# Kernel tuning notes

Measured on AMD Instinct MI355X. Metric: run time of the kernel, lower is better.

Reference implementation:

```python
import jax, jax.numpy as jnp
import numpy as np

IN_SIZE = 1024
OUT_SIZE = 4096
LOGN = 12          # ceil(log2(max(in,out)))
N = 1 << LOGN      # 4096
BATCH = 8192


def setup_inputs() -> dict:
    key = jax.random.key(0)
    k1, k2, k3 = jax.random.split(key, 3)
    # kaiming_uniform on [2*logN, N]: fan_in = N, bound = sqrt(6/fan_in)
    bound = float(np.sqrt(6.0 / N))
    learned_params = jax.random.uniform(k1, (2 * LOGN, N), minval=-bound, maxval=bound, dtype=jnp.float32)
    inp = jax.random.normal(k2, (BATCH, IN_SIZE), dtype=jnp.float32)
    # np.random.permutation(N)[:out_size]
    out_row_indices = jax.random.permutation(k3, N)[:OUT_SIZE].astype(jnp.int32)
    return {"input": inp, "learned_params": learned_params, "out_row_indices": out_row_indices}


def reference(input, learned_params, out_row_indices):
    # Build B = prod_i (diag(p[2i]) + P_i @ diag(p[2i+1])), P_i[j, j^2^i] = 1.
    # (P_i @ diag(d) @ B)[j, :] = d[j^2^i] * B[j^2^i, :], so each layer is a
    # row-scale + xor-permuted row-scale of B (same math as the dense matmul chain).
    B = jnp.eye(N, dtype=input.dtype)
    for i in range(LOGN):
        perm = jnp.arange(N) ^ (1 << i)  # static per layer
        B = learned_params[2 * i][:, None] * B + learned_params[2 * i + 1][perm][:, None] * B[perm]
    layer_matrix = B[out_row_indices, :IN_SIZE]   # [out_size, in_size]
    return input @ layer_matrix.T                  # [batch, out_size]
```

## Files before the change

### kernel.cpp

```cpp
#include <hip/hip_runtime.h>


typedef float f4 __attribute__((ext_vector_type(4)));
typedef float f2 __attribute__((ext_vector_type(2)));
typedef int   i4 __attribute__((ext_vector_type(4)));

__device__ __forceinline__ int swz(int e) {
    return e ^ (((e >> 5) & 3) << 2);
}

template<int CTRL>
__device__ __forceinline__ float dppx(float x) {
    int xi = __builtin_bit_cast(int, x);
    int r  = __builtin_amdgcn_update_dpp(xi, xi, CTRL, 0xF, 0xF, true);
    return __builtin_bit_cast(float, r);
}

#if __has_builtin(__builtin_amdgcn_permlane16_swap) && __has_builtin(__builtin_amdgcn_permlane32_swap)
#define HAVE_PERMLANE_SWAP 1
__device__ __forceinline__ float xswap16(float x) {
    unsigned xi = __builtin_bit_cast(unsigned, x);
    auto r = __builtin_amdgcn_permlane16_swap(xi, xi, false, false);
    return __builtin_bit_cast(float, r[0] ^ r[1] ^ xi);
}
__device__ __forceinline__ float xswap32(float x) {
    unsigned xi = __builtin_bit_cast(unsigned, x);
    auto r = __builtin_amdgcn_permlane32_swap(xi, xi, false, false);
    return __builtin_bit_cast(float, r[0] ^ r[1] ^ xi);
}
#else
#define HAVE_PERMLANE_SWAP 0
__device__ __forceinline__ float xswap16(float x) { return __shfl_xor(x, 16, 64); }
__device__ __forceinline__ float xswap32(float x) { return __shfl_xor(x, 32, 64); }
#endif

__global__ void __launch_bounds__(256) bfly_prep(
    const float* __restrict__ lp, const int* __restrict__ orow,
    float* __restrict__ scale, int* __restrict__ src2)
{
    int j = blockIdx.x * 256 + threadIdx.x;
    if (j >= 4096) return;
    int r = orow[j];
    int c = r & 1023;
    int u = r & 2047;
    const float* A10 = lp + 20 * 4096;
    const float* B10 = lp + 21 * 4096;
    const float* A11 = lp + 22 * 4096;
    const float* B11 = lp + 23 * 4096;
    float f11 = (r & 2048) ? B11[u] : A11[u];
    float f10 = (r & 1024) ? B10[c] : A10[c];
    scale[j] = f11 * f10;
    src2[j] = c ^ (((c >> 4) & 7) << 1);
}

__global__ void __launch_bounds__(512, 2) bfly_main(
    const float* __restrict__ inp, const float* __restrict__ lp,
    const float* __restrict__ scale, const int* __restrict__ src2,
    float* __restrict__ out)
{
    __shared__ __align__(16) float cf[20 * 1024 + 8 * 2048];
    const int t = threadIdx.x;
    const int wave = t >> 6, lane = t & 63;

    #pragma unroll
    for (int step = 0; step < 10; ++step) {
        const int q = 2 * step + (t >> 8);
        const int e = (t & 255) * 4;
        const f4 v = *reinterpret_cast<const f4*>(lp + (size_t)q * 4096 + e);
        *reinterpret_cast<f4*>(&cf[q * 1024 + swz(e)]) = v;
    }

    const int sBase = blockIdx.x * 16 + wave * 2;
    float x[2][16];
    #pragma unroll
    for (int m = 0; m < 2; ++m) {
        const f4* p = reinterpret_cast<const f4*>(inp + (size_t)(sBase + m) * 1024 + lane * 16);
        #pragma unroll
        for (int c = 0; c < 4; ++c) {
            f4 v = p[c];
            x[m][4*c+0] = v.x; x[m][4*c+1] = v.y; x[m][4*c+2] = v.z; x[m][4*c+3] = v.w;
        }
    }

    __syncthreads();

    #pragma unroll
    for (int i = 0; i < 2; ++i) {
        const float* arow = &cf[(size_t)(2*i)     * 1024];
        const float* brow = &cf[(size_t)(2*i + 1) * 1024];
        #pragma unroll
        for (int c = 0; c < 4; ++c) {
            f4 va = *reinterpret_cast<const f4*>(&arow[swz(lane * 16 + 4 * c)]);
            f4 vb = *reinterpret_cast<const f4*>(&brow[swz(lane * 16 + 4 * c)]);
            #pragma unroll
            for (int m = 0; m < 2; ++m) {
                float* xm = x[m];
                if (i == 0) {
                    float lo0 = xm[4*c+0], hi0 = xm[4*c+1];
                    xm[4*c+0] = va[0] * lo0 + vb[1] * hi0;
                    xm[4*c+1] = va[1] * hi0 + vb[0] * lo0;
                    float lo1 = xm[4*c+2], hi1 = xm[4*c+3];
                    xm[4*c+2] = va[2] * lo1 + vb[3] * hi1;
                    xm[4*c+3] = va[3] * hi1 + vb[2] * lo1;
                } else {
                    float lo0 = xm[4*c+0], hi0 = xm[4*c+2];
                    xm[4*c+0] = va[0] * lo0 + vb[2] * hi0;
                    xm[4*c+2] = va[2] * hi0 + vb[0] * lo0;
                    float lo1 = xm[4*c+1], hi1 = xm[4*c+3];
                    xm[4*c+1] = va[1] * lo1 + vb[3] * hi1;
                    xm[4*c+3] = va[3] * hi1 + vb[1] * lo1;
                }
            }
        }
    }

    #pragma unroll
    for (int i = 2; i < 4; ++i) {
        const float* arow = &cf[(size_t)(2*i)     * 1024];
        const float* brow = &cf[(size_t)(2*i + 1) * 1024];
        #pragma unroll
        for (int g = 0; g < 2; ++g) {
            const int q0 = (i == 2) ? 2 * g : g;
            const int q1 = (i == 2) ? q0 + 1 : q0 + 2;
            f4 va0 = *reinterpret_cast<const f4*>(&arow[swz(lane * 16 + 4 * q0)]);
            f4 va1 = *reinterpret_cast<const f4*>(&arow[swz(lane * 16 + 4 * q1)]);
            f4 vb0 = *reinterpret_cast<const f4*>(&brow[swz(lane * 16 + 4 * q0)]);
            f4 vb1 = *reinterpret_cast<const f4*>(&brow[swz(lane * 16 + 4 * q1)]);
            #pragma unroll
            for (int m = 0; m < 2; ++m) {
                float* xm = x[m];
                #pragma unroll
                for (int e = 0; e < 4; ++e) {
                    float lo = xm[4*q0+e], hi = xm[4*q1+e];
                    xm[4*q0+e] = va0[e] * lo + vb1[e] * hi;
                    xm[4*q1+e] = va1[e] * hi + vb0[e] * lo;
                }
            }
        }
    }

    {
        const float* arow = &cf[(size_t)8 * 1024];
        const float* brow = &cf[(size_t)9 * 1024];
        #pragma unroll
        for (int c = 0; c < 4; ++c) {
            f4 va = *reinterpret_cast<const f4*>(&arow[swz(lane * 16 + 4 * c)]);
            f4 vb = *reinterpret_cast<const f4*>(&brow[swz((lane ^ 1) * 16 + 4 * c)]);
            #pragma unroll
            for (int m = 0; m < 2; ++m) {
                #pragma unroll
                for (int e = 0; e < 4; ++e) {
                    float v = x[m][4*c+e];
                    x[m][4*c+e] = va[e] * v + vb[e] * dppx<0xB1>(v);
                }
            }
        }
    }

    #pragma unroll
    for (int i = 5; i < 10; ++i) {
        const int d = 1 << (i - 4);
        const float* arow = &cf[(size_t)(2*i)     * 1024];
        const float* brow = &cf[(size_t)(2*i + 1) * 1024];
        #pragma unroll
        for (int c = 0; c < 4; ++c) {
            f4 va = *reinterpret_cast<const f4*>(&arow[swz(lane * 16 + 4 * c)]);
            f4 vb = *reinterpret_cast<const f4*>(&brow[swz((lane ^ d) * 16 + 4 * c)]);
            #pragma unroll
            for (int m = 0; m < 2; ++m) {
                #pragma unroll
                for (int e = 0; e < 4; ++e) {
                    float v = x[m][4*c+e];
                    float xp = (d == 2)  ? dppx<0x4E>(v)
                             : (d == 8)  ? dppx<0x128>(v)
                             : (d == 16) ? xswap16(v)
                             : (d == 32) ? xswap32(v)
                             :             __shfl_xor(v, d, 64);
                    x[m][4*c+e] = va[e] * v + vb[e] * xp;
                }
            }
        }
    }

    float* zz = &cf[20 * 1024 + (size_t)wave * 2048];
    const int km0 = (lane & 7) << 1;
    #pragma unroll
    for (int k = 0; k < 16; k += 2) {
        int pi = lane * 16 + (k ^ km0);
        f4 v = { x[0][k], x[1][k], x[0][k+1], x[1][k+1] };
        *reinterpret_cast<f4*>(&zz[2 * pi]) = v;
    }

    const i4* srv = reinterpret_cast<const i4*>(src2);
    const f4* scv = reinterpret_cast<const f4*>(scale);
    f4* o0 = reinterpret_cast<f4*>(out + (size_t)sBase * 4096);
    f4* o1 = reinterpret_cast<f4*>(out + (size_t)(sBase + 1) * 4096);

    i4 si = srv[lane];
    f4 sc = scv[lane];
    #pragma unroll
    for (int it = 0; it < 16; ++it) {
        i4 si_c = si;
        f4 sc_c = sc;
        if (it + 1 < 16) {
            si = srv[(it + 1) * 64 + lane];
            sc = scv[(it + 1) * 64 + lane];
        }
        int j4 = it * 64 + lane;
        f2 vx = *reinterpret_cast<const f2*>(&zz[2 * si_c.x]);
        f2 vy = *reinterpret_cast<const f2*>(&zz[2 * si_c.y]);
        f2 vz = *reinterpret_cast<const f2*>(&zz[2 * si_c.z]);
        f2 vw = *reinterpret_cast<const f2*>(&zz[2 * si_c.w]);
        f4 r0 = { sc_c.x * vx.x, sc_c.y * vy.x, sc_c.z * vz.x, sc_c.w * vw.x };
        f4 r1 = { sc_c.x * vx.y, sc_c.y * vy.y, sc_c.z * vz.y, sc_c.w * vw.y };
        o0[j4] = r0;
        o1[j4] = r1;
    }
}

extern "C" void kernel_launch(void* const* d_in, const int* in_sizes, int n_in,
                              void* d_out, int out_size, void* d_ws, size_t ws_size,
                              hipStream_t stream) {
    const float* inp  = (const float*)d_in[0];
    const float* lp   = (const float*)d_in[1];
    const int*   orow = (const int*)d_in[2];
    float* out = (float*)d_out;

    float* scale = (float*)d_ws;
    int*   src2  = (int*)((char*)d_ws + 4096 * 4);

    bfly_prep<<<16, 256, 0, stream>>>(lp, orow, scale, src2);
    bfly_main<<<512, 512, 0, stream>>>(inp, lp, scale, src2, out);
}
```

Baseline: 41.76 us.

## Process four rows per wave with 256-thread blocks and f4 gather staging

After: 46.16 us. 1.11x slower.

```diff
diff --git a/kernel.cpp b/kernel.cpp
--- a/kernel.cpp
+++ b/kernel.cpp
@@ -2,7 +2,6 @@
 
 
 typedef float f4 __attribute__((ext_vector_type(4)));
-typedef float f2 __attribute__((ext_vector_type(2)));
 typedef int   i4 __attribute__((ext_vector_type(4)));
 
 __device__ __forceinline__ int swz(int e) {
@@ -17,7 +16,6 @@
 }
 
 #if __has_builtin(__builtin_amdgcn_permlane16_swap) && __has_builtin(__builtin_amdgcn_permlane32_swap)
-#define HAVE_PERMLANE_SWAP 1
 __device__ __forceinline__ float xswap16(float x) {
     unsigned xi = __builtin_bit_cast(unsigned, x);
     auto r = __builtin_amdgcn_permlane16_swap(xi, xi, false, false);
@@ -29,14 +27,13 @@
     return __builtin_bit_cast(float, r[0] ^ r[1] ^ xi);
 }
 #else
-#define HAVE_PERMLANE_SWAP 0
 __device__ __forceinline__ float xswap16(float x) { return __shfl_xor(x, 16, 64); }
 __device__ __forceinline__ float xswap32(float x) { return __shfl_xor(x, 32, 64); }
 #endif
 
 __global__ void __launch_bounds__(256) bfly_prep(
     const float* __restrict__ lp, const int* __restrict__ orow,
-    float* __restrict__ scale, int* __restrict__ src2)
+    float* __restrict__ scale, int* __restrict__ src4)
 {
     int j = blockIdx.x * 256 + threadIdx.x;
     if (j >= 4096) return;
@@ -50,30 +47,29 @@
     float f11 = (r & 2048) ? B11[u] : A11[u];
     float f10 = (r & 1024) ? B10[c] : A10[c];
     scale[j] = f11 * f10;
-    src2[j] = c ^ (((c >> 4) & 7) << 1);
-}
-
-__global__ void __launch_bounds__(512, 2) bfly_main(
+    src4[j] = c ^ ((c >> 4) & 7);
+}
+
+__global__ void __launch_bounds__(256, 1) bfly_main(
     const float* __restrict__ inp, const float* __restrict__ lp,
-    const float* __restrict__ scale, const int* __restrict__ src2,
+    const float* __restrict__ scale, const int* __restrict__ src4,
     float* __restrict__ out)
 {
-    __shared__ __align__(16) float cf[20 * 1024 + 8 * 2048];
+    __shared__ __align__(16) float cf[20 * 1024 + 4 * 4096];
     const int t = threadIdx.x;
     const int wave = t >> 6, lane = t & 63;
 
     #pragma unroll
-    for (int step = 0; step < 10; ++step) {
-        const int q = 2 * step + (t >> 8);
-        const int e = (t & 255) * 4;
+    for (int q = 0; q < 20; ++q) {
+        const int e = t * 4;
         const f4 v = *reinterpret_cast<const f4*>(lp + (size_t)q * 4096 + e);
         *reinterpret_cast<f4*>(&cf[q * 1024 + swz(e)]) = v;
     }
 
-    const int sBase = blockIdx.x * 16 + wave * 2;
-    float x[2][16];
-    #pragma unroll
-    for (int m = 0; m < 2; ++m) {
+    const int sBase = blockIdx.x * 16 + wave * 4;
+    float x[4][16];
+    #pragma unroll
+    for (int m = 0; m < 4; ++m) {
         const f4* p = reinterpret_cast<const f4*>(inp + (size_t)(sBase + m) * 1024 + lane * 16);
         #pragma unroll
         for (int c = 0; c < 4; ++c) {
@@ -93,7 +89,7 @@
             f4 va = *reinterpret_cast<const f4*>(&arow[swz(lane * 16 + 4 * c)]);
             f4 vb = *reinterpret_cast<const f4*>(&brow[swz(lane * 16 + 4 * c)]);
             #pragma unroll
-            for (int m = 0; m < 2; ++m) {
+            for (int m = 0; m < 4; ++m) {
                 float* xm = x[m];
                 if (i == 0) {
                     float lo0 = xm[4*c+0], hi0 = xm[4*c+1];
@@ -127,7 +123,7 @@
             f4 vb0 = *reinterpret_cast<const f4*>(&brow[swz(lane * 16 + 4 * q0)]);
             f4 vb1 = *reinterpret_cast<const f4*>(&brow[swz(lane * 16 + 4 * q1)]);
             #pragma unroll
-            for (int m = 0; m < 2; ++m) {
+            for (int m = 0; m < 4; ++m) {
                 float* xm = x[m];
                 #pragma unroll
                 for (int e = 0; e < 4; ++e) {
@@ -147,7 +143,7 @@
             f4 va = *reinterpret_cast<const f4*>(&arow[swz(lane * 16 + 4 * c)]);
             f4 vb = *reinterpret_cast<const f4*>(&brow[swz((lane ^ 1) * 16 + 4 * c)]);
             #pragma unroll
-            for (int m = 0; m < 2; ++m) {
+            for (int m = 0; m < 4; ++m) {
                 #pragma unroll
                 for (int e = 0; e < 4; ++e) {
                     float v = x[m][4*c+e];
@@ -167,7 +163,7 @@
             f4 va = *reinterpret_cast<const f4*>(&arow[swz(lane * 16 + 4 * c)]);
             f4 vb = *reinterpret_cast<const f4*>(&brow[swz((lane ^ d) * 16 + 4 * c)]);
             #pragma unroll
-            for (int m = 0; m < 2; ++m) {
+            for (int m = 0; m < 4; ++m) {
                 #pragma unroll
                 for (int e = 0; e < 4; ++e) {
                     float v = x[m][4*c+e];
@@ -182,19 +178,20 @@
         }
     }
 
-    float* zz = &cf[20 * 1024 + (size_t)wave * 2048];
-    const int km0 = (lane & 7) << 1;
-    #pragma unroll
-    for (int k = 0; k < 16; k += 2) {
-        int pi = lane * 16 + (k ^ km0);
-        f4 v = { x[0][k], x[1][k], x[0][k+1], x[1][k+1] };
-        *reinterpret_cast<f4*>(&zz[2 * pi]) = v;
-    }
-
-    const i4* srv = reinterpret_cast<const i4*>(src2);
+    f4* zz = reinterpret_cast<f4*>(&cf[20 * 1024]) + (size_t)wave * 1024;
+    const int km = lane & 7;
+    #pragma unroll
+    for (int k = 0; k < 16; ++k) {
+        f4 v = { x[0][k], x[1][k], x[2][k], x[3][k] };
+        zz[(lane * 16 + k) ^ km] = v;
+    }
+
+    const i4* srv = reinterpret_cast<const i4*>(src4);
     const f4* scv = reinterpret_cast<const f4*>(scale);
-    f4* o0 = reinterpret_cast<f4*>(out + (size_t)sBase * 4096);
+    f4* o0 = reinterpret_cast<f4*>(out + (size_t)(sBase + 0) * 4096);
     f4* o1 = reinterpret_cast<f4*>(out + (size_t)(sBase + 1) * 4096);
+    f4* o2 = reinterpret_cast<f4*>(out + (size_t)(sBase + 2) * 4096);
+    f4* o3 = reinterpret_cast<f4*>(out + (size_t)(sBase + 3) * 4096);
 
     i4 si = srv[lane];
     f4 sc = scv[lane];
@@ -207,14 +204,18 @@
             sc = scv[(it + 1) * 64 + lane];
         }
         int j4 = it * 64 + lane;
-        f2 vx = *reinterpret_cast<const f2*>(&zz[2 * si_c.x]);
-        f2 vy = *reinterpret_cast<const f2*>(&zz[2 * si_c.y]);
-        f2 vz = *reinterpret_cast<const f2*>(&zz[2 * si_c.z]);
-        f2 vw = *reinterpret_cast<const f2*>(&zz[2 * si_c.w]);
-        f4 r0 = { sc_c.x * vx.x, sc_c.y * vy.x, sc_c.z * vz.x, sc_c.w * vw.x };
-        f4 r1 = { sc_c.x * vx.y, sc_c.y * vy.y, sc_c.z * vz.y, sc_c.w * vw.y };
+        f4 vx = zz[si_c.x];
+        f4 vy = zz[si_c.y];
+        f4 vz = zz[si_c.z];
+        f4 vw = zz[si_c.w];
+        f4 r0 = { sc_c.x * vx[0], sc_c.y * vy[0], sc_c.z * vz[0], sc_c.w * vw[0] };
+        f4 r1 = { sc_c.x * vx[1], sc_c.y * vy[1], sc_c.z * vz[1], sc_c.w * vw[1] };
+        f4 r2 = { sc_c.x * vx[2], sc_c.y * vy[2], sc_c.z * vz[2], sc_c.w * vw[2] };
+        f4 r3 = { sc_c.x * vx[3], sc_c.y * vy[3], sc_c.z * vz[3], sc_c.w * vw[3] };
         o0[j4] = r0;
         o1[j4] = r1;
+        o2[j4] = r2;
+        o3[j4] = r3;
     }
 }
 
@@ -227,8 +228,8 @@
     float* out = (float*)d_out;
 
     float* scale = (float*)d_ws;
-    int*   src2  = (int*)((char*)d_ws + 4096 * 4);
-
-    bfly_prep<<<16, 256, 0, stream>>>(lp, orow, scale, src2);
-    bfly_main<<<512, 512, 0, stream>>>(inp, lp, scale, src2, out);
-}
+    int*   src4  = (int*)((char*)d_ws + 4096 * 4);
+
+    bfly_prep<<<16, 256, 0, stream>>>(lp, orow, scale, src4);
+    bfly_main<<<512, 256, 0, stream>>>(inp, lp, scale, src4, out);
+}
```
